# Kernel tuning notes

Hardware: AMD Instinct MI355X
Metric: run time of the kernel (lower is better)

## Reference

```python
import jax, jax.numpy as jnp
import numpy as np


def setup_inputs() -> dict:
    key = jax.random.key(0)
    kx, kc = jax.random.split(key)
    N, K, D = 32768, 4096, 512
    x = jax.random.normal(kx, (N, D), dtype=jnp.float32)
    # matches torch.rand(K, D) * 0.2 - 0.1
    codebook = jax.random.uniform(kc, (K, D), dtype=jnp.float32) * 0.2 - 0.1
    return {"x": x, "codebook": codebook}


def reference(x, codebook):
    x_sq = jnp.sum(x * x, axis=-1, keepdims=True)            # [N, 1]
    c_sq = jnp.sum(codebook * codebook, axis=-1)             # [K]
    dists = x_sq - 2.0 * jnp.einsum('nd,kd->nk', x, codebook) + c_sq[None, :]
    Z = jnp.argmin(dists, axis=-1)                           # [N] int
    q = codebook[Z]                                          # [N, D] gather
    q_with_st = x + jax.lax.stop_gradient(q - x)             # straight-through
    vq_loss = jnp.mean((jax.lax.stop_gradient(q) - x) ** 2)
    commitment_loss = jnp.mean((jax.lax.stop_gradient(x) - q) ** 2)
    return Z, q_with_st, vq_loss, commitment_loss
```

## Files before the change

### kernel.cpp

```cpp
#include <hip/hip_runtime.h>

static constexpr int N = 32768;
static constexpr int K = 4096;
static constexpr int D = 512;

typedef _Float16 f16x8 __attribute__((ext_vector_type(8)));
typedef float f32x4 __attribute__((ext_vector_type(4)));

#define GLD16(GP, LP)                                                   \
  __builtin_amdgcn_global_load_lds(                                     \
      (const __attribute__((address_space(1))) void*)(GP),              \
      (__attribute__((address_space(3))) void*)(LP), 16, 0, 0)

__global__ void rowsq_kernel(const float* __restrict__ a, float* __restrict__ out,
                             int rows) {
  int tid = threadIdx.x;
  int row = blockIdx.x * 8 + (tid >> 5);
  if (row >= rows) return;
  int l = tid & 31;
  const float* p = a + (size_t)row * D + (l >> 3) * 128 + (l & 7);
  float r = 0.f;
#pragma unroll
  for (int i = 0; i < 16; ++i) {
    float v = p[i * 8];
    r = __fadd_rn(r, __fmul_rn(v, v));
  }
  r = __fadd_rn(r, __shfl_xor(r, 1));
  r = __fadd_rn(r, __shfl_xor(r, 2));
  r = __fadd_rn(r, __shfl_xor(r, 4));
  r = __fadd_rn(r, __shfl_xor(r, 8));
  r = __fadd_rn(r, __shfl_xor(r, 16));
  if (l == 0) out[row] = r;
}

__global__ __launch_bounds__(256) void convert_hi_kernel(
    const float* __restrict__ in, _Float16* __restrict__ hi, float scale,
    size_t n8) {
  for (size_t i = (size_t)blockIdx.x * 256 + threadIdx.x; i < n8;
       i += (size_t)gridDim.x * 256) {
    const float4* p = (const float4*)(in + i * 8);
    float4 a = p[0], b = p[1];
    float s[8] = {a.x, a.y, a.z, a.w, b.x, b.y, b.z, b.w};
    union { _Float16 h[8]; f16x8 v; } H;
#pragma unroll
    for (int j = 0; j < 8; ++j) H.h[j] = (_Float16)(s[j] * scale);
    *(f16x8*)(hi + i * 8) = H.v;
  }
}

__global__ __launch_bounds__(256) void transpose_kernel(
    const float* __restrict__ in, float* __restrict__ outT) {
  __shared__ float t[32][33];
  int bk = blockIdx.x;
  int bd = blockIdx.y;
  int tx = threadIdx.x, ty = threadIdx.y;
#pragma unroll
  for (int j = 0; j < 32; j += 8)
    t[ty + j][tx] = in[(size_t)(bk * 32 + ty + j) * D + bd * 32 + tx];
  __syncthreads();
#pragma unroll
  for (int j = 0; j < 32; j += 8)
    outT[(size_t)(bd * 32 + ty + j) * K + bk * 32 + tx] = t[tx][ty + j];
}

__global__ __launch_bounds__(256) void mfma_argmin_kernel(
    const _Float16* __restrict__ xh, const _Float16* __restrict__ ch,
    const float* __restrict__ xsq, const float* __restrict__ csq,
    float* __restrict__ pv1, int* __restrict__ pi1, float* __restrict__ pv2) {
  __shared__ __align__(16) _Float16 Ah[2][128 * 32];
  __shared__ __align__(16) _Float16 Bh[2][128 * 32];
  __shared__ float mbv1[128];
  __shared__ int mbi1[128];
  __shared__ float mbv2[128];

  int bid = blockIdx.x;
  int xcd = bid & 7, j = bid >> 3;
  int rowPanel = xcd * 32 + (j >> 5);
  int colPanel = j & 31;

  int tid = threadIdx.x;
  int w = tid >> 6, l = tid & 63;
  int wr = w >> 1, wc = w & 1;
  int wrow = wr * 64, wcol = wc * 64;
  int rA = l & 15, g = l >> 4;

  const size_t rowBase = (size_t)rowPanel * 128;
  const size_t colBase = (size_t)colPanel * 128;

  f32x4 acc[4][4];
#pragma unroll
  for (int mi = 0; mi < 4; ++mi)
#pragma unroll
    for (int ni = 0; ni < 4; ++ni) acc[mi][ni] = (f32x4)0.f;

  const int r0 = tid >> 2, s0 = tid & 3;
  const int cs = s0 ^ ((r0 >> 1) & 3);
  const int swz = (g ^ ((rA >> 1) & 3)) * 8;

  const _Float16* aSrc = xh + (rowBase + r0) * D + cs * 8;
  const _Float16* bSrc = ch + (colBase + r0) * D + cs * 8;

  auto stage = [&](int buf, int kt) {
    const int dOff = kt * 32;
    GLD16(aSrc + dOff, &Ah[buf][(size_t)tid * 8]);
    GLD16(aSrc + dOff + (size_t)64 * D, &Ah[buf][(size_t)(tid + 256) * 8]);
    GLD16(bSrc + dOff, &Bh[buf][(size_t)tid * 8]);
    GLD16(bSrc + dOff + (size_t)64 * D, &Bh[buf][(size_t)(tid + 256) * 8]);
  };

  stage(0, 0);
  int cur = 0;
  for (int kt = 0; kt < 16; ++kt) {
    __syncthreads();
    if (kt < 15) stage(cur ^ 1, kt + 1);

    f16x8 ah[4], bh[4];
#pragma unroll
    for (int f = 0; f < 4; ++f) {
      ah[f] = *(const f16x8*)&Ah[cur][(wrow + f * 16 + rA) * 32 + swz];
      bh[f] = *(const f16x8*)&Bh[cur][(wcol + f * 16 + rA) * 32 + swz];
    }
#pragma unroll
    for (int mi = 0; mi < 4; ++mi)
#pragma unroll
      for (int ni = 0; ni < 4; ++ni)
        acc[mi][ni] =
            __builtin_amdgcn_mfma_f32_16x16x32_f16(ah[mi], bh[ni], acc[mi][ni], 0, 0, 0);
    cur ^= 1;
  }

  const float inv2048 = 1.0f / 2048.0f;
  float fv1[4][4], fv2[4][4];
  int fi1[4][4];
#pragma unroll
  for (int mi = 0; mi < 4; ++mi) {
#pragma unroll
    for (int r = 0; r < 4; ++r) {
      int row_l = wrow + mi * 16 + g * 4 + r;
      float xq = xsq[rowBase + row_l];
      float bv1 = 1e30f, bv2 = 1e30f;
      int bi1 = 0x7fffffff;
#pragma unroll
      for (int ni = 0; ni < 4; ++ni) {
        int col = (int)colBase + wcol + ni * 16 + rA;
        float S = acc[mi][ni][r];
        float dsc = (xq - S * inv2048) + csq[col];
        if (dsc < bv1 || (dsc == bv1 && col < bi1)) {
          bv2 = bv1; bv1 = dsc; bi1 = col;
        } else if (dsc < bv2) {
          bv2 = dsc;
        }
      }
#pragma unroll
      for (int m = 1; m < 16; m <<= 1) {
        float ov1 = __shfl_xor(bv1, m);
        int oi1 = __shfl_xor(bi1, m);
        float ov2 = __shfl_xor(bv2, m);
        if (ov1 < bv1 || (ov1 == bv1 && oi1 < bi1)) {
          bv2 = fminf(bv1, ov2); bv1 = ov1; bi1 = oi1;
        } else {
          bv2 = fminf(bv2, ov1);
        }
      }
      fv1[mi][r] = bv1; fv2[mi][r] = bv2; fi1[mi][r] = bi1;
      if (wc == 1 && rA == 0) {
        mbv1[row_l] = bv1; mbi1[row_l] = bi1; mbv2[row_l] = bv2;
      }
    }
  }
  __syncthreads();
  if (wc == 0 && rA == 0) {
#pragma unroll
    for (int mi = 0; mi < 4; ++mi) {
#pragma unroll
      for (int r = 0; r < 4; ++r) {
        int row_l = wrow + mi * 16 + g * 4 + r;
        float bv1 = fv1[mi][r], bv2 = fv2[mi][r];
        int bi1 = fi1[mi][r];
        float ov1 = mbv1[row_l];
        int oi1 = mbi1[row_l];
        float ov2 = mbv2[row_l];
        if (ov1 < bv1 || (ov1 == bv1 && oi1 < bi1)) {
          bv2 = fminf(bv1, ov2); bv1 = ov1; bi1 = oi1;
        } else {
          bv2 = fminf(bv2, ov1);
        }
        size_t o = (size_t)colPanel * N + (rowBase + row_l);
        pv1[o] = bv1; pi1[o] = bi1; pv2[o] = bv2;
      }
    }
  }
}

__global__ __launch_bounds__(256) void reduce_kernel(
    const float* __restrict__ pv1, const int* __restrict__ pi1,
    const float* __restrict__ pv2, float* __restrict__ zout,
    int* __restrict__ ctr, int* __restrict__ list, float eps) {
  int row = blockIdx.x * 256 + threadIdx.x;
  if (row >= N) return;
  float v1 = 1e30f, v2 = 1e30f;
  int i1 = 0x7fffffff;
  for (int jj = 0; jj < 32; ++jj) {
    float ov1 = pv1[(size_t)jj * N + row];
    float ov2 = pv2[(size_t)jj * N + row];
    int oi1 = pi1[(size_t)jj * N + row];
    if (ov1 < v1 || (ov1 == v1 && oi1 < i1)) {
      v2 = fminf(v1, ov2); v1 = ov1; i1 = oi1;
    } else {
      v2 = fminf(v2, ov1);
    }
  }
  zout[row] = (float)i1;
  if (v2 - v1 < eps) {
    int p = atomicAdd(ctr, 1);
    if (p < N) list[p] = row;
  }
}

static constexpr int RT_ROWS = 16;
static constexpr int RT_PANELS = 8;
static constexpr int CHUNK_D = 8;

__global__ __launch_bounds__(256) void rescore_tiled_kernel(
    const float* __restrict__ x, const float* __restrict__ cbT,
    const float* __restrict__ xsq, const float* __restrict__ csq,
    const int* __restrict__ ctr, const int* __restrict__ list,
    float* __restrict__ prv, int* __restrict__ pri) {
  __shared__ float xs[RT_ROWS][D + 4];
  __shared__ __align__(16) float cbs[2][CHUNK_D][512];
  int cnt = *ctr;
  if (cnt > N) cnt = N;
  int nTiles = (cnt + RT_ROWS - 1) / RT_ROWS;
  int nItems = nTiles * RT_PANELS;
  int tid = threadIdx.x;
  int ty = tid >> 4;
  int tx = tid & 15;

  for (int item = blockIdx.x; item < nItems; item += gridDim.x) {
    int tileIdx = item >> 3;
    int panel = item & 7;
    int base = tileIdx * RT_ROWS;
    int colPanel = panel * 512;
    __syncthreads();

    for (int i = tid; i < RT_ROWS * (D / 4); i += 256) {
      int r = i >> 7;
      int d4 = i & 127;
      int fi = base + r;
      int row = list[fi < cnt ? fi : 0];
      ((float4*)&xs[r][0])[d4] = ((const float4*)(x + (size_t)row * D))[d4];
    }

    auto stageCb = [&](int buf, int chk) {
      const float* src = cbT + (size_t)(chk * CHUNK_D) * K + colPanel;
#pragma unroll
      for (int it = 0; it < 4; ++it) {
        int f = it * 256 + tid;
        int dd = f >> 7, c4 = f & 127;
        GLD16(src + (size_t)dd * K + c4 * 4, &cbs[buf][0][0] + (size_t)f * 4);
      }
    };

    stageCb(0, 0);
    float acc[32];
#pragma unroll
    for (int c = 0; c < 32; ++c) acc[c] = 0.f;

    int cur = 0;
    for (int chk = 0; chk < D / CHUNK_D; ++chk) {
      __syncthreads();
      if (chk < D / CHUNK_D - 1) stageCb(cur ^ 1, chk + 1);
#pragma unroll
      for (int dd = 0; dd < CHUNK_D; ++dd) {
        float xa = xs[ty][chk * CHUNK_D + dd];
        const float4* cp = (const float4*)&cbs[cur][dd][0];
#pragma unroll
        for (int jj = 0; jj < 8; ++jj) {
          float4 v = cp[tx + jj * 16];
          acc[jj * 4 + 0] = fmaf(xa, v.x, acc[jj * 4 + 0]);
          acc[jj * 4 + 1] = fmaf(xa, v.y, acc[jj * 4 + 1]);
          acc[jj * 4 + 2] = fmaf(xa, v.z, acc[jj * 4 + 2]);
          acc[jj * 4 + 3] = fmaf(xa, v.w, acc[jj * 4 + 3]);
        }
      }
      cur ^= 1;
    }

    int fi = base + ty;
    int row = list[fi < cnt ? fi : 0];
    float xq = xsq[row];
    float bv = 1e30f;
    int bi = 0x7fffffff;
#pragma unroll
    for (int jj = 0; jj < 8; ++jj) {
#pragma unroll
      for (int q = 0; q < 4; ++q) {
        int col = colPanel + jj * 64 + tx * 4 + q;
        float a = acc[jj * 4 + q];
        float two = __fadd_rn(a, a);
        float t = __fsub_rn(xq, two);
        float dsc = __fadd_rn(t, csq[col]);
        if (dsc < bv || (dsc == bv && col < bi)) { bv = dsc; bi = col; }
      }
    }
#pragma unroll
    for (int m = 1; m < 16; m <<= 1) {
      float ov = __shfl_xor(bv, m);
      int oi = __shfl_xor(bi, m);
      if (ov < bv || (ov == bv && oi < bi)) { bv = ov; bi = oi; }
    }
    if (tx == 0 && fi < cnt) {
      prv[(size_t)fi * RT_PANELS + panel] = bv;
      pri[(size_t)fi * RT_PANELS + panel] = bi;
    }
  }
}

__global__ __launch_bounds__(256) void rescore_reduce_kernel(
    const float* __restrict__ prv, const int* __restrict__ pri,
    const int* __restrict__ ctr, const int* __restrict__ list,
    float* __restrict__ zout) {
  int cnt = *ctr;
  if (cnt > N) cnt = N;
  for (int fi = blockIdx.x * 256 + threadIdx.x; fi < cnt;
       fi += gridDim.x * 256) {
    float bv = 1e30f;
    int bi = 0x7fffffff;
#pragma unroll
    for (int p = 0; p < RT_PANELS; ++p) {
      float v = prv[(size_t)fi * RT_PANELS + p];
      int i = pri[(size_t)fi * RT_PANELS + p];
      if (v < bv || (v == bv && i < bi)) { bv = v; bi = i; }
    }
    zout[list[fi]] = (float)bi;
  }
}

static constexpr int BM = 64;
static constexpr int BKc = 128;
static constexpr int BD = 32;

__global__ __launch_bounds__(256) void argmin_fp32_kernel(
    const float* __restrict__ x, const float* __restrict__ cb,
    const float* __restrict__ xsq, const float* __restrict__ csq,
    float* __restrict__ zout) {
  __shared__ float xs[BD][BM];
  __shared__ float cs_[BD][BKc];
  __shared__ float mv[BM][16];
  __shared__ int mi[BM][16];

  int tid = threadIdx.x;
  int tx = tid & 15;
  int ty = tid >> 4;
  int row0 = blockIdx.x * BM;

  float bestv[4];
  int besti[4];
  float xsqr[4];
#pragma unroll
  for (int i = 0; i < 4; ++i) {
    bestv[i] = 3.4e38f;
    besti[i] = 0x7fffffff;
    xsqr[i] = xsq[row0 + ty * 4 + i];
  }

  for (int kt = 0; kt < K; kt += BKc) {
    float acc[4][8];
#pragma unroll
    for (int i = 0; i < 4; ++i)
#pragma unroll
      for (int jj = 0; jj < 8; ++jj) acc[i][jj] = 0.f;

    for (int dt = 0; dt < D; dt += BD) {
      __syncthreads();
      {
        int r = tid >> 2, d0 = (tid & 3) * 8;
        const float* src = x + (size_t)(row0 + r) * D + dt + d0;
        float4 v0 = *(const float4*)(src);
        float4 v1 = *(const float4*)(src + 4);
        xs[d0 + 0][r] = v0.x; xs[d0 + 1][r] = v0.y;
        xs[d0 + 2][r] = v0.z; xs[d0 + 3][r] = v0.w;
        xs[d0 + 4][r] = v1.x; xs[d0 + 5][r] = v1.y;
        xs[d0 + 6][r] = v1.z; xs[d0 + 7][r] = v1.w;
      }
      {
        int kk = tid >> 1, d0 = (tid & 1) * 16;
        const float* src = cb + (size_t)(kt + kk) * D + dt + d0;
        float4 v0 = *(const float4*)(src);
        float4 v1 = *(const float4*)(src + 4);
        float4 v2 = *(const float4*)(src + 8);
        float4 v3 = *(const float4*)(src + 12);
        cs_[d0 + 0][kk] = v0.x;  cs_[d0 + 1][kk] = v0.y;
        cs_[d0 + 2][kk] = v0.z;  cs_[d0 + 3][kk] = v0.w;
        cs_[d0 + 4][kk] = v1.x;  cs_[d0 + 5][kk] = v1.y;
        cs_[d0 + 6][kk] = v1.z;  cs_[d0 + 7][kk] = v1.w;
        cs_[d0 + 8][kk] = v2.x;  cs_[d0 + 9][kk] = v2.y;
        cs_[d0 + 10][kk] = v2.z; cs_[d0 + 11][kk] = v2.w;
        cs_[d0 + 12][kk] = v3.x; cs_[d0 + 13][kk] = v3.y;
        cs_[d0 + 14][kk] = v3.z; cs_[d0 + 15][kk] = v3.w;
      }
      __syncthreads();
#pragma unroll 4
      for (int d = 0; d < BD; ++d) {
        float xa[4], cv[8];
        *(float4*)&xa[0] = *(const float4*)&xs[d][ty * 4];
        *(float4*)&cv[0] = *(const float4*)&cs_[d][tx * 8];
        *(float4*)&cv[4] = *(const float4*)&cs_[d][tx * 8 + 4];
#pragma unroll
        for (int i = 0; i < 4; ++i)
#pragma unroll
          for (int jj = 0; jj < 8; ++jj)
            acc[i][jj] = fmaf(xa[i], cv[jj], acc[i][jj]);
      }
    }

#pragma unroll
    for (int jj = 0; jj < 8; ++jj) {
      int k = kt + tx * 8 + jj;
      float cq = csq[k];
#pragma unroll
      for (int i = 0; i < 4; ++i) {
        float two = __fadd_rn(acc[i][jj], acc[i][jj]);
        float t = __fsub_rn(xsqr[i], two);
        float dsc = __fadd_rn(t, cq);
        if (dsc < bestv[i]) { bestv[i] = dsc; besti[i] = k; }
      }
    }
  }

  __syncthreads();
#pragma unroll
  for (int i = 0; i < 4; ++i) {
    mv[ty * 4 + i][tx] = bestv[i];
    mi[ty * 4 + i][tx] = besti[i];
  }
  __syncthreads();
  if (tid < BM) {
    float bv = mv[tid][0];
    int bi = mi[tid][0];
#pragma unroll
    for (int t = 1; t < 16; ++t) {
      float v = mv[tid][t];
      int ii = mi[tid][t];
      if (v < bv || (v == bv && ii < bi)) { bv = v; bi = ii; }
    }
    zout[row0 + tid] = (float)bi;
  }
}

__global__ __launch_bounds__(256) void gather_kernel(
    const float* __restrict__ x, const float* __restrict__ cb,
    const float* __restrict__ zf, float* __restrict__ qout,
    float* __restrict__ partial) {
  __shared__ float red[256];
  const size_t TOT4 = (size_t)N * D / 4;
  size_t t0 = (size_t)blockIdx.x * 256 + threadIdx.x;
  float lsum = 0.f;
  for (size_t f = t0; f < TOT4; f += (size_t)2048 * 256) {
    int n = (int)(f >> 7);
    int d4 = (int)(f & 127);
    int z = (int)zf[n];
    float4 xv = ((const float4*)x)[f];
    float4 qv = *(const float4*)(cb + (size_t)z * D + d4 * 4);
    float dx0 = __fsub_rn(qv.x, xv.x);
    float dx1 = __fsub_rn(qv.y, xv.y);
    float dx2 = __fsub_rn(qv.z, xv.z);
    float dx3 = __fsub_rn(qv.w, xv.w);
    float4 o;
    o.x = __fadd_rn(xv.x, dx0);
    o.y = __fadd_rn(xv.y, dx1);
    o.z = __fadd_rn(xv.z, dx2);
    o.w = __fadd_rn(xv.w, dx3);
    ((float4*)qout)[f] = o;
    lsum += dx0 * dx0 + dx1 * dx1 + dx2 * dx2 + dx3 * dx3;
  }
  red[threadIdx.x] = lsum;
  __syncthreads();
  for (int s = 128; s > 0; s >>= 1) {
    if (threadIdx.x < s) red[threadIdx.x] += red[threadIdx.x + s];
    __syncthreads();
  }
  if (threadIdx.x == 0) partial[blockIdx.x] = red[0];
}

__global__ __launch_bounds__(256) void loss_kernel(const float* __restrict__ partial,
                                                   float* __restrict__ loss_out) {
  __shared__ float red[256];
  float s = 0.f;
  for (int i = threadIdx.x; i < 2048; i += 256) s += partial[i];
  red[threadIdx.x] = s;
  __syncthreads();
  for (int k = 128; k > 0; k >>= 1) {
    if (threadIdx.x < k) red[threadIdx.x] += red[threadIdx.x + k];
    __syncthreads();
  }
  if (threadIdx.x == 0) {
    float m = red[0] / (float)((size_t)N * D);
    loss_out[0] = m;
    loss_out[1] = m;
  }
}

static constexpr size_t OFF_XSQ = 0;
static constexpr size_t OFF_CSQ = 131072;
static constexpr size_t OFF_PART = 147456;
static constexpr size_t OFF_CTR = 155648;
static constexpr size_t OFF_LIST = 155904;
static constexpr size_t OFF_PV1 = 286976;
static constexpr size_t OFF_PI1 = OFF_PV1 + 4194304;
static constexpr size_t OFF_PV2 = OFF_PI1 + 4194304;
static constexpr size_t OFF_PRV = OFF_PV2 + 4194304;
static constexpr size_t OFF_PRI = OFF_PRV + 1048576;
static constexpr size_t OFF_CHI = OFF_PRI + 1048576;
static constexpr size_t WS_REQ = OFF_CHI + 4194304;

extern "C" void kernel_launch(void* const* d_in, const int* in_sizes, int n_in,
                              void* d_out, int out_size, void* d_ws, size_t ws_size,
                              hipStream_t stream) {
  const float* x = (const float*)d_in[0];
  const float* cb = (const float*)d_in[1];
  float* out = (float*)d_out;

  float* zout = out;
  float* qout = out + N;
  float* lout = out + N + (size_t)N * D;

  char* ws = (char*)d_ws;
  float* xsq = (float*)(ws + OFF_XSQ);
  float* csq = (float*)(ws + OFF_CSQ);
  float* partial = (float*)(ws + OFF_PART);

  rowsq_kernel<<<dim3(N / 8), dim3(256), 0, stream>>>(x, xsq, N);
  rowsq_kernel<<<dim3(K / 8), dim3(256), 0, stream>>>(cb, csq, K);

  if (ws_size >= WS_REQ) {
    int* ctr = (int*)(ws + OFF_CTR);
    int* list = (int*)(ws + OFF_LIST);
    float* pv1 = (float*)(ws + OFF_PV1);
    int* pi1 = (int*)(ws + OFF_PI1);
    float* pv2 = (float*)(ws + OFF_PV2);
    float* prv = (float*)(ws + OFF_PRV);
    int* pri = (int*)(ws + OFF_PRI);
    _Float16* chi = (_Float16*)(ws + OFF_CHI);

    _Float16* xhi = (_Float16*)qout;
    float* cbT = (float*)((char*)qout + (size_t)N * D * 2);

    convert_hi_kernel<<<dim3(2048), dim3(256), 0, stream>>>(x, xhi, 16.0f,
                                                            (size_t)N * D / 8);
    convert_hi_kernel<<<dim3(1024), dim3(256), 0, stream>>>(cb, chi, 256.0f,
                                                            (size_t)K * D / 8);
    transpose_kernel<<<dim3(K / 32, D / 32), dim3(32, 8), 0, stream>>>(cb, cbT);
    hipMemsetAsync(ctr, 0, sizeof(int), stream);
    mfma_argmin_kernel<<<dim3((N / 128) * (K / 128)), dim3(256), 0, stream>>>(
        xhi, chi, xsq, csq, pv1, pi1, pv2);
    reduce_kernel<<<dim3(N / 256), dim3(256), 0, stream>>>(pv1, pi1, pv2, zout,
                                                           ctr, list, 0.02f);
    rescore_tiled_kernel<<<dim3(1024), dim3(256), 0, stream>>>(
        x, cbT, xsq, csq, ctr, list, prv, pri);
    rescore_reduce_kernel<<<dim3(128), dim3(256), 0, stream>>>(prv, pri, ctr,
                                                               list, zout);
  } else {
    argmin_fp32_kernel<<<dim3(N / BM), dim3(256), 0, stream>>>(x, cb, xsq, csq,
                                                               zout);
  }

  gather_kernel<<<dim3(2048), dim3(256), 0, stream>>>(x, cb, zout, qout, partial);
  loss_kernel<<<dim3(1), dim3(256), 0, stream>>>(partial, lout);
}
```

Measured before the change: 557.3 us.

## Enlarge MFMA argmin tile to 256x256 with 8-wave ping-pong pipelined staging

The fp16 MFMA distance/argmin kernel moves from 128x128 tiles with 4 waves to 256x256 tiles with 8 waves. Each wave now computes 128x64, and loads of the next k-slice are split into halves placed between explicit barriers, with s_setprio raised around the MFMA bursts. The aim is more data reuse per LDS load, fewer global reads of x and the codebook, and half as many partial results for the reduce kernel. The cost is larger accumulators (128 floats per lane), which cuts occupancy, plus extra barriers per k-step.

```diff
diff --git a/kernel.cpp b/kernel.cpp
--- a/kernel.cpp
+++ b/kernel.cpp
@@ -11,6 +11,8 @@
   __builtin_amdgcn_global_load_lds(                                     \
       (const __attribute__((address_space(1))) void*)(GP),              \
       (__attribute__((address_space(3))) void*)(LP), 16, 0, 0)
+
+#define FENCE asm volatile("" ::: "memory")
 
 __global__ void rowsq_kernel(const float* __restrict__ a, float* __restrict__ out,
                              int rows) {
@@ -63,87 +65,125 @@
     outT[(size_t)(bd * 32 + ty + j) * K + bk * 32 + tx] = t[tx][ty + j];
 }
 
-__global__ __launch_bounds__(256) void mfma_argmin_kernel(
+__global__ __launch_bounds__(512, 2) void mfma_argmin_kernel(
     const _Float16* __restrict__ xh, const _Float16* __restrict__ ch,
     const float* __restrict__ xsq, const float* __restrict__ csq,
     float* __restrict__ pv1, int* __restrict__ pi1, float* __restrict__ pv2) {
-  __shared__ __align__(16) _Float16 Ah[2][128 * 32];
-  __shared__ __align__(16) _Float16 Bh[2][128 * 32];
-  __shared__ float mbv1[128];
-  __shared__ int mbi1[128];
-  __shared__ float mbv2[128];
+  __shared__ __align__(16) _Float16 AB[2][2][256][32];
+  __shared__ float emv1[256][4];
+  __shared__ float emv2[256][4];
+  __shared__ int emi1[256][4];
 
   int bid = blockIdx.x;
   int xcd = bid & 7, j = bid >> 3;
-  int rowPanel = xcd * 32 + (j >> 5);
-  int colPanel = j & 31;
+  int rowPanel = xcd * 16 + (j >> 4);
+  int colPanel = j & 15;
 
   int tid = threadIdx.x;
-  int w = tid >> 6, l = tid & 63;
-  int wr = w >> 1, wc = w & 1;
-  int wrow = wr * 64, wcol = wc * 64;
+  int wid = tid >> 6, l = tid & 63;
+  int wr = wid >> 2, wcn = wid & 3;
   int rA = l & 15, g = l >> 4;
-
-  const size_t rowBase = (size_t)rowPanel * 128;
-  const size_t colBase = (size_t)colPanel * 128;
-
-  f32x4 acc[4][4];
-#pragma unroll
-  for (int mi = 0; mi < 4; ++mi)
-#pragma unroll
-    for (int ni = 0; ni < 4; ++ni) acc[mi][ni] = (f32x4)0.f;
-
-  const int r0 = tid >> 2, s0 = tid & 3;
-  const int cs = s0 ^ ((r0 >> 1) & 3);
   const int swz = (g ^ ((rA >> 1) & 3)) * 8;
 
-  const _Float16* aSrc = xh + (rowBase + r0) * D + cs * 8;
-  const _Float16* bSrc = ch + (colBase + r0) * D + cs * 8;
-
-  auto stage = [&](int buf, int kt) {
-    const int dOff = kt * 32;
-    GLD16(aSrc + dOff, &Ah[buf][(size_t)tid * 8]);
-    GLD16(aSrc + dOff + (size_t)64 * D, &Ah[buf][(size_t)(tid + 256) * 8]);
-    GLD16(bSrc + dOff, &Bh[buf][(size_t)tid * 8]);
-    GLD16(bSrc + dOff + (size_t)64 * D, &Bh[buf][(size_t)(tid + 256) * 8]);
+  const size_t rowBase = (size_t)rowPanel * 256;
+  const size_t colBase = (size_t)colPanel * 256;
+
+  f32x4 acc[8][4];
+#pragma unroll
+  for (int m = 0; m < 8; ++m)
+#pragma unroll
+    for (int n = 0; n < 4; ++n) acc[m][n] = (f32x4)0.f;
+
+  const int srow = tid >> 2;
+  const int kc = tid & 3;
+  const int kcs = (kc ^ ((srow >> 1) & 3)) * 8;
+
+  auto stageHalf = [&](int buf, int mat, int half, int kt) {
+    const _Float16* src =
+        (mat == 0 ? xh + (rowBase + half * 128 + srow) * D
+                  : ch + (colBase + half * 128 + srow) * D) +
+        kt * 32 + kcs;
+    GLD16(src, (_Float16*)&AB[buf][mat][0][0] + half * 4096 + tid * 8);
   };
-
-  stage(0, 0);
+  auto ldA = [&](int cur, int fm) {
+    return *(const f16x8*)(&AB[cur][0][wr * 128 + fm * 16 + rA][0] + swz);
+  };
+  auto ldB = [&](int cur, int fn) {
+    return *(const f16x8*)(&AB[cur][1][wcn * 64 + fn * 16 + rA][0] + swz);
+  };
+
+  stageHalf(0, 0, 0, 0);
+  stageHalf(0, 0, 1, 0);
+  stageHalf(0, 1, 0, 0);
+  stageHalf(0, 1, 1, 0);
+  asm volatile("s_waitcnt vmcnt(0)" ::: "memory");
+  FENCE;
+  __builtin_amdgcn_s_barrier();
+  FENCE;
+
   int cur = 0;
   for (int kt = 0; kt < 16; ++kt) {
-    __syncthreads();
-    if (kt < 15) stage(cur ^ 1, kt + 1);
-
-    f16x8 ah[4], bh[4];
-#pragma unroll
-    for (int f = 0; f < 4; ++f) {
-      ah[f] = *(const f16x8*)&Ah[cur][(wrow + f * 16 + rA) * 32 + swz];
-      bh[f] = *(const f16x8*)&Bh[cur][(wcol + f * 16 + rA) * 32 + swz];
-    }
-#pragma unroll
-    for (int mi = 0; mi < 4; ++mi)
-#pragma unroll
-      for (int ni = 0; ni < 4; ++ni)
-        acc[mi][ni] =
-            __builtin_amdgcn_mfma_f32_16x16x32_f16(ah[mi], bh[ni], acc[mi][ni], 0, 0, 0);
+    f16x8 bh[4], ah[4];
+#pragma unroll
+    for (int n = 0; n < 4; ++n) bh[n] = ldB(cur, n);
+#pragma unroll
+    for (int m = 0; m < 4; ++m) ah[m] = ldA(cur, m);
+    if (kt < 15) {
+      stageHalf(cur ^ 1, 0, 0, kt + 1);
+      stageHalf(cur ^ 1, 0, 1, kt + 1);
+    }
+    FENCE;
+    __builtin_amdgcn_s_barrier();
+    FENCE;
+    __builtin_amdgcn_s_setprio(1);
+#pragma unroll
+    for (int n = 0; n < 4; ++n)
+#pragma unroll
+      for (int m = 0; m < 4; ++m)
+        acc[m][n] =
+            __builtin_amdgcn_mfma_f32_16x16x32_f16(ah[m], bh[n], acc[m][n], 0, 0, 0);
+    __builtin_amdgcn_s_setprio(0);
+    FENCE;
+    __builtin_amdgcn_s_barrier();
+    FENCE;
+    f16x8 ah2[4];
+#pragma unroll
+    for (int m = 0; m < 4; ++m) ah2[m] = ldA(cur, 4 + m);
+    if (kt < 15) {
+      stageHalf(cur ^ 1, 1, 0, kt + 1);
+      stageHalf(cur ^ 1, 1, 1, kt + 1);
+    }
+    FENCE;
+    __builtin_amdgcn_s_barrier();
+    FENCE;
+    __builtin_amdgcn_s_setprio(1);
+#pragma unroll
+    for (int n = 0; n < 4; ++n)
+#pragma unroll
+      for (int m = 0; m < 4; ++m)
+        acc[4 + m][n] =
+            __builtin_amdgcn_mfma_f32_16x16x32_f16(ah2[m], bh[n], acc[4 + m][n], 0, 0, 0);
+    __builtin_amdgcn_s_setprio(0);
+    asm volatile("s_waitcnt vmcnt(0)" ::: "memory");
+    FENCE;
+    __builtin_amdgcn_s_barrier();
+    FENCE;
     cur ^= 1;
   }
 
   const float inv2048 = 1.0f / 2048.0f;
-  float fv1[4][4], fv2[4][4];
-  int fi1[4][4];
-#pragma unroll
-  for (int mi = 0; mi < 4; ++mi) {
-#pragma unroll
-    for (int r = 0; r < 4; ++r) {
-      int row_l = wrow + mi * 16 + g * 4 + r;
+#pragma unroll
+  for (int fm = 0; fm < 8; ++fm) {
+#pragma unroll
+    for (int rr = 0; rr < 4; ++rr) {
+      int row_l = wr * 128 + fm * 16 + g * 4 + rr;
       float xq = xsq[rowBase + row_l];
       float bv1 = 1e30f, bv2 = 1e30f;
       int bi1 = 0x7fffffff;
 #pragma unroll
-      for (int ni = 0; ni < 4; ++ni) {
-        int col = (int)colBase + wcol + ni * 16 + rA;
-        float S = acc[mi][ni][r];
+      for (int fn = 0; fn < 4; ++fn) {
+        int col = (int)colBase + wcn * 64 + fn * 16 + rA;
+        float S = acc[fm][fn][rr];
         float dsc = (xq - S * inv2048) + csq[col];
         if (dsc < bv1 || (dsc == bv1 && col < bi1)) {
           bv2 = bv1; bv1 = dsc; bi1 = col;
@@ -162,33 +202,30 @@
           bv2 = fminf(bv2, ov1);
         }
       }
-      fv1[mi][r] = bv1; fv2[mi][r] = bv2; fi1[mi][r] = bi1;
-      if (wc == 1 && rA == 0) {
-        mbv1[row_l] = bv1; mbi1[row_l] = bi1; mbv2[row_l] = bv2;
+      if (rA == 0) {
+        emv1[row_l][wcn] = bv1;
+        emi1[row_l][wcn] = bi1;
+        emv2[row_l][wcn] = bv2;
       }
     }
   }
   __syncthreads();
-  if (wc == 0 && rA == 0) {
-#pragma unroll
-    for (int mi = 0; mi < 4; ++mi) {
-#pragma unroll
-      for (int r = 0; r < 4; ++r) {
-        int row_l = wrow + mi * 16 + g * 4 + r;
-        float bv1 = fv1[mi][r], bv2 = fv2[mi][r];
-        int bi1 = fi1[mi][r];
-        float ov1 = mbv1[row_l];
-        int oi1 = mbi1[row_l];
-        float ov2 = mbv2[row_l];
-        if (ov1 < bv1 || (ov1 == bv1 && oi1 < bi1)) {
-          bv2 = fminf(bv1, ov2); bv1 = ov1; bi1 = oi1;
-        } else {
-          bv2 = fminf(bv2, ov1);
-        }
-        size_t o = (size_t)colPanel * N + (rowBase + row_l);
-        pv1[o] = bv1; pi1[o] = bi1; pv2[o] = bv2;
-      }
-    }
+  if (tid < 256) {
+    float bv1 = emv1[tid][0], bv2 = emv2[tid][0];
+    int bi1 = emi1[tid][0];
+#pragma unroll
+    for (int p = 1; p < 4; ++p) {
+      float ov1 = emv1[tid][p];
+      int oi1 = emi1[tid][p];
+      float ov2 = emv2[tid][p];
+      if (ov1 < bv1 || (ov1 == bv1 && oi1 < bi1)) {
+        bv2 = fminf(bv1, ov2); bv1 = ov1; bi1 = oi1;
+      } else {
+        bv2 = fminf(bv2, ov1);
+      }
+    }
+    size_t o = (size_t)colPanel * N + (rowBase + tid);
+    pv1[o] = bv1; pi1[o] = bi1; pv2[o] = bv2;
   }
 }
 
@@ -200,7 +237,7 @@
   if (row >= N) return;
   float v1 = 1e30f, v2 = 1e30f;
   int i1 = 0x7fffffff;
-  for (int jj = 0; jj < 32; ++jj) {
+  for (int jj = 0; jj < 16; ++jj) {
     float ov1 = pv1[(size_t)jj * N + row];
     float ov2 = pv2[(size_t)jj * N + row];
     int oi1 = pi1[(size_t)jj * N + row];
@@ -507,9 +544,9 @@
 static constexpr size_t OFF_CTR = 155648;
 static constexpr size_t OFF_LIST = 155904;
 static constexpr size_t OFF_PV1 = 286976;
-static constexpr size_t OFF_PI1 = OFF_PV1 + 4194304;
-static constexpr size_t OFF_PV2 = OFF_PI1 + 4194304;
-static constexpr size_t OFF_PRV = OFF_PV2 + 4194304;
+static constexpr size_t OFF_PI1 = OFF_PV1 + 2097152;
+static constexpr size_t OFF_PV2 = OFF_PI1 + 2097152;
+static constexpr size_t OFF_PRV = OFF_PV2 + 2097152;
 static constexpr size_t OFF_PRI = OFF_PRV + 1048576;
 static constexpr size_t OFF_CHI = OFF_PRI + 1048576;
 static constexpr size_t WS_REQ = OFF_CHI + 4194304;
@@ -552,7 +589,7 @@
                                                             (size_t)K * D / 8);
     transpose_kernel<<<dim3(K / 32, D / 32), dim3(32, 8), 0, stream>>>(cb, cbT);
     hipMemsetAsync(ctr, 0, sizeof(int), stream);
-    mfma_argmin_kernel<<<dim3((N / 128) * (K / 128)), dim3(256), 0, stream>>>(
+    mfma_argmin_kernel<<<dim3((N / 256) * (K / 256)), dim3(512), 0, stream>>>(
         xhi, chi, xsq, csq, pv1, pi1, pv2);
     reduce_kernel<<<dim3(N / 256), dim3(256), 0, stream>>>(pv1, pi1, pv2, zout,
                                                            ctr, list, 0.02f);
```

Result: slower. 574.4 us (+3.1%).

## Fuse row-norm with fp16 conversion and load A operand directly to registers

Applied to the files above, without the earlier changes.

Merges the row-squared-norm and fp16 conversion passes into one kernel that reads each input row once, staging it through shared memory for the norm reduction. The MFMA argmin kernel stops staging the x tile in LDS and has each lane load its A fragments straight from global memory into registers, prefetching the next k-slice. The codebook fp16 copy moves out of the workspace into spare output space, and the k-loop is fully unrolled. This cuts kernel launches and LDS traffic, but direct global A loads are less coalesced and use more registers.

```diff
diff --git a/kernel.cpp b/kernel.cpp
--- a/kernel.cpp
+++ b/kernel.cpp
@@ -12,13 +12,32 @@
       (const __attribute__((address_space(1))) void*)(GP),              \
       (__attribute__((address_space(3))) void*)(LP), 16, 0, 0)
 
-__global__ void rowsq_kernel(const float* __restrict__ a, float* __restrict__ out,
-                             int rows) {
+__global__ __launch_bounds__(256) void rowsq_convert_kernel(
+    const float* __restrict__ in, float* __restrict__ sqout,
+    _Float16* __restrict__ hi, float scale, int rows) {
+  __shared__ float ls[8][512];
+  int rb = blockIdx.x * 8;
   int tid = threadIdx.x;
-  int row = blockIdx.x * 8 + (tid >> 5);
-  if (row >= rows) return;
+#pragma unroll
+  for (int g2 = 0; g2 < 2; ++g2) {
+    int g = g2 * 256 + tid;
+    int r = g >> 6;
+    int c8 = (g & 63) * 8;
+    const float4* p = (const float4*)(in + (size_t)(rb + r) * D + c8);
+    float4 a = p[0], b = p[1];
+    float s[8] = {a.x, a.y, a.z, a.w, b.x, b.y, b.z, b.w};
+    union { _Float16 h[8]; f16x8 v; } H;
+#pragma unroll
+    for (int jj = 0; jj < 8; ++jj) {
+      H.h[jj] = (_Float16)(s[jj] * scale);
+      ls[r][c8 + jj] = s[jj];
+    }
+    *(f16x8*)(hi + (size_t)(rb + r) * D + c8) = H.v;
+  }
+  __syncthreads();
+  int rr = tid >> 5;
   int l = tid & 31;
-  const float* p = a + (size_t)row * D + (l >> 3) * 128 + (l & 7);
+  const float* p = &ls[rr][(l >> 3) * 128 + (l & 7)];
   float r = 0.f;
 #pragma unroll
   for (int i = 0; i < 16; ++i) {
@@ -30,22 +49,7 @@
   r = __fadd_rn(r, __shfl_xor(r, 4));
   r = __fadd_rn(r, __shfl_xor(r, 8));
   r = __fadd_rn(r, __shfl_xor(r, 16));
-  if (l == 0) out[row] = r;
-}
-
-__global__ __launch_bounds__(256) void convert_hi_kernel(
-    const float* __restrict__ in, _Float16* __restrict__ hi, float scale,
-    size_t n8) {
-  for (size_t i = (size_t)blockIdx.x * 256 + threadIdx.x; i < n8;
-       i += (size_t)gridDim.x * 256) {
-    const float4* p = (const float4*)(in + i * 8);
-    float4 a = p[0], b = p[1];
-    float s[8] = {a.x, a.y, a.z, a.w, b.x, b.y, b.z, b.w};
-    union { _Float16 h[8]; f16x8 v; } H;
-#pragma unroll
-    for (int j = 0; j < 8; ++j) H.h[j] = (_Float16)(s[j] * scale);
-    *(f16x8*)(hi + i * 8) = H.v;
-  }
+  if (l == 0) sqout[rb + rr] = r;
 }
 
 __global__ __launch_bounds__(256) void transpose_kernel(
@@ -67,7 +71,6 @@
     const _Float16* __restrict__ xh, const _Float16* __restrict__ ch,
     const float* __restrict__ xsq, const float* __restrict__ csq,
     float* __restrict__ pv1, int* __restrict__ pi1, float* __restrict__ pv2) {
-  __shared__ __align__(16) _Float16 Ah[2][128 * 32];
   __shared__ __align__(16) _Float16 Bh[2][128 * 32];
   __shared__ float mbv1[128];
   __shared__ int mbi1[128];
@@ -96,36 +99,48 @@
   const int r0 = tid >> 2, s0 = tid & 3;
   const int cs = s0 ^ ((r0 >> 1) & 3);
   const int swz = (g ^ ((rA >> 1) & 3)) * 8;
-
-  const _Float16* aSrc = xh + (rowBase + r0) * D + cs * 8;
   const _Float16* bSrc = ch + (colBase + r0) * D + cs * 8;
 
-  auto stage = [&](int buf, int kt) {
+  auto stageB = [&](int buf, int kt) {
     const int dOff = kt * 32;
-    GLD16(aSrc + dOff, &Ah[buf][(size_t)tid * 8]);
-    GLD16(aSrc + dOff + (size_t)64 * D, &Ah[buf][(size_t)(tid + 256) * 8]);
     GLD16(bSrc + dOff, &Bh[buf][(size_t)tid * 8]);
     GLD16(bSrc + dOff + (size_t)64 * D, &Bh[buf][(size_t)(tid + 256) * 8]);
   };
 
-  stage(0, 0);
+  const _Float16* aRow[4];
+#pragma unroll
+  for (int f = 0; f < 4; ++f)
+    aRow[f] = xh + (rowBase + wrow + f * 16 + rA) * D + g * 8;
+
+  f16x8 aCur[4], aNext[4];
+  stageB(0, 0);
+#pragma unroll
+  for (int f = 0; f < 4; ++f) aCur[f] = *(const f16x8*)(aRow[f]);
+
   int cur = 0;
+#pragma unroll
   for (int kt = 0; kt < 16; ++kt) {
     __syncthreads();
-    if (kt < 15) stage(cur ^ 1, kt + 1);
-
-    f16x8 ah[4], bh[4];
-#pragma unroll
-    for (int f = 0; f < 4; ++f) {
-      ah[f] = *(const f16x8*)&Ah[cur][(wrow + f * 16 + rA) * 32 + swz];
+    if (kt < 15) {
+      stageB(cur ^ 1, kt + 1);
+#pragma unroll
+      for (int f = 0; f < 4; ++f)
+        aNext[f] = *(const f16x8*)(aRow[f] + (kt + 1) * 32);
+    }
+    f16x8 bh[4];
+#pragma unroll
+    for (int f = 0; f < 4; ++f)
       bh[f] = *(const f16x8*)&Bh[cur][(wcol + f * 16 + rA) * 32 + swz];
-    }
 #pragma unroll
     for (int mi = 0; mi < 4; ++mi)
 #pragma unroll
       for (int ni = 0; ni < 4; ++ni)
         acc[mi][ni] =
-            __builtin_amdgcn_mfma_f32_16x16x32_f16(ah[mi], bh[ni], acc[mi][ni], 0, 0, 0);
+            __builtin_amdgcn_mfma_f32_16x16x32_f16(aCur[mi], bh[ni], acc[mi][ni], 0, 0, 0);
+    if (kt < 15) {
+#pragma unroll
+      for (int f = 0; f < 4; ++f) aCur[f] = aNext[f];
+    }
     cur ^= 1;
   }
 
@@ -511,8 +526,7 @@
 static constexpr size_t OFF_PV2 = OFF_PI1 + 4194304;
 static constexpr size_t OFF_PRV = OFF_PV2 + 4194304;
 static constexpr size_t OFF_PRI = OFF_PRV + 1048576;
-static constexpr size_t OFF_CHI = OFF_PRI + 1048576;
-static constexpr size_t WS_REQ = OFF_CHI + 4194304;
+static constexpr size_t WS_REQ = OFF_PRI + 1048576;
 
 extern "C" void kernel_launch(void* const* d_in, const int* in_sizes, int n_in,
                               void* d_out, int out_size, void* d_ws, size_t ws_size,
@@ -530,8 +544,14 @@
   float* csq = (float*)(ws + OFF_CSQ);
   float* partial = (float*)(ws + OFF_PART);
 
-  rowsq_kernel<<<dim3(N / 8), dim3(256), 0, stream>>>(x, xsq, N);
-  rowsq_kernel<<<dim3(K / 8), dim3(256), 0, stream>>>(cb, csq, K);
+  _Float16* xhi = (_Float16*)qout;
+  float* cbT = (float*)((char*)qout + (size_t)N * D * 2);
+  _Float16* chi = (_Float16*)((char*)cbT + (size_t)D * K * 4);
+
+  rowsq_convert_kernel<<<dim3(N / 8), dim3(256), 0, stream>>>(x, xsq, xhi,
+                                                              16.0f, N);
+  rowsq_convert_kernel<<<dim3(K / 8), dim3(256), 0, stream>>>(cb, csq, chi,
+                                                              256.0f, K);
 
   if (ws_size >= WS_REQ) {
     int* ctr = (int*)(ws + OFF_CTR);
@@ -541,15 +561,7 @@
     float* pv2 = (float*)(ws + OFF_PV2);
     float* prv = (float*)(ws + OFF_PRV);
     int* pri = (int*)(ws + OFF_PRI);
-    _Float16* chi = (_Float16*)(ws + OFF_CHI);
-
-    _Float16* xhi = (_Float16*)qout;
-    float* cbT = (float*)((char*)qout + (size_t)N * D * 2);
-
-    convert_hi_kernel<<<dim3(2048), dim3(256), 0, stream>>>(x, xhi, 16.0f,
-                                                            (size_t)N * D / 8);
-    convert_hi_kernel<<<dim3(1024), dim3(256), 0, stream>>>(cb, chi, 256.0f,
-                                                            (size_t)K * D / 8);
+
     transpose_kernel<<<dim3(K / 32, D / 32), dim3(32, 8), 0, stream>>>(cb, cbT);
     hipMemsetAsync(ctr, 0, sizeof(int), stream);
     mfma_argmin_kernel<<<dim3((N / 128) * (K / 128)), dim3(256), 0, stream>>>(
```

Result: slower. 644.8 us (+15.7%).
